# Kernel tuning notes

Measured on AMD Instinct MI355X. Metric: run time of the kernel, lower is better.

Reference implementation:

```python
import jax, jax.numpy as jnp
import numpy as np

NUM_Q = 50000
DIM_KEY = 128
DIM_VALUE = 256
DIM_HIDDEN = 512
MEM_SIZE = 50
BATCH = 128
SEQ = 2048


def setup_inputs() -> dict:
    key = jax.random.key(0)
    ks = jax.random.split(key, 12)
    inp = {
        "q": jax.random.randint(ks[0], (BATCH, SEQ), 0, NUM_Q + 1, dtype=jnp.int64 if jax.config.jax_enable_x64 else jnp.int32),
        "a": jax.random.randint(ks[1], (BATCH, SEQ), 0, 2, dtype=jnp.int64 if jax.config.jax_enable_x64 else jnp.int32),
        # learned parameters (torch Linear convention: y = x @ W.T + b)
        "key_memory": jax.random.normal(ks[2], (MEM_SIZE, DIM_KEY), jnp.float32) * 0.1,
        "value_memory": jax.random.normal(ks[3], (MEM_SIZE, DIM_VALUE), jnp.float32) * 0.1,
        "embed_table": jax.random.normal(ks[4], (NUM_Q + 1, DIM_KEY), jnp.float32) * 0.1,
        "W_erase": jax.random.normal(ks[5], (DIM_VALUE, DIM_HIDDEN), jnp.float32) * 0.05,
        "b_erase": jnp.zeros((DIM_VALUE,), jnp.float32),
        "W_add": jax.random.normal(ks[6], (DIM_VALUE, DIM_HIDDEN), jnp.float32) * 0.05,
        "b_add": jnp.zeros((DIM_VALUE,), jnp.float32),
        "W_f": jax.random.normal(ks[7], (DIM_HIDDEN, DIM_VALUE + DIM_KEY), jnp.float32) * 0.05,
        "b_f": jnp.zeros((DIM_HIDDEN,), jnp.float32),
        "W_p": jax.random.normal(ks[8], (1, DIM_HIDDEN), jnp.float32) * 0.05,
        "b_p": jnp.zeros((1,), jnp.float32),
    }
    return inp


def reference(q, a, key_memory, value_memory, embed_table, W_erase, b_erase,
              W_add, b_add, W_f, b_f, W_p, b_p):
    # NOTE: in the original torch module, read() always uses the static
    # value_memory parameter (not the per-batch updated memory), and the
    # answer sequence `a` is never used in the forward math. Hence the
    # timestep loop is embarrassingly parallel and we vectorize over t.
    q_embed = embed_table[q]                                   # [B,S,K]
    corr = jax.nn.softmax(jnp.einsum('bsk,mk->bsm', q_embed, key_memory), axis=-1)  # [B,S,M]
    read_content = jnp.einsum('bsm,mv->bsv', corr, value_memory)                    # [B,S,V]
    feat = jnp.concatenate([read_content, q_embed], axis=-1)   # [B,S,V+K]
    # dropout is identity in eval mode
    state = jax.nn.relu(jnp.einsum('bsf,hf->bsh', feat, W_f) + b_f)                 # [B,S,H]
    pred = jax.nn.sigmoid(jnp.einsum('bsh,oh->bso', state, W_p) + b_p)              # [B,S,1]
    return pred[..., 0]                                        # [B,S]
```

## Files before the change

### kernel.cpp

```cpp
#include <hip/hip_runtime.h>
#include <hip/hip_bf16.h>

#define NUM_Q_MAX 50000
#define DIM_KEY 128
#define DIM_VAL 256
#define WF_COLS 384
#define DIM_HID 512
#define MEMN    50
#define KDIM    192
#define EOFF    56
#define PITCH   200
#define QB      64

typedef __bf16 bf16x8 __attribute__((ext_vector_type(8)));
typedef float  f32x4  __attribute__((ext_vector_type(4)));
union Frag { uint4 u; bf16x8 b; };

__device__ __forceinline__ float blo(unsigned u){ return __uint_as_float(u << 16); }
__device__ __forceinline__ float bhi(unsigned u){ return __uint_as_float(u & 0xffff0000u); }
__device__ __forceinline__ unsigned short f2b(float x){
    unsigned u = __float_as_uint(x);
    u += 0x7fffu + ((u >> 16) & 1u);
    return (unsigned short)(u >> 16);
}
__device__ __forceinline__ unsigned pk2(float a, float b){
    return (unsigned)f2b(a) | ((unsigned)f2b(b) << 16);
}

__global__ void __launch_bounds__(64)
prep_kernel(const float* __restrict__ Wf, const float* __restrict__ Vm,
            const float* __restrict__ Kmem,
            unsigned short* __restrict__ WCt, unsigned short* __restrict__ Kbt){
    const int b = blockIdx.x, t = threadIdx.x;
    if (b < DIM_HID) {
        const int h = b, nt = h >> 4, l15 = h & 15;
        for (int j = t; j < KDIM; j += 64) {
            float val = 0.f;
            if (j < MEMN) {
                const float4* wr = (const float4*)(Wf + h * WF_COLS);
                const float4* vr = (const float4*)(Vm + j * DIM_VAL);
                float s = 0.f;
                for (int v = 0; v < DIM_VAL / 4; ++v) {
                    float4 a = wr[v], c = vr[v];
                    s += a.x*c.x + a.y*c.y + a.z*c.z + a.w*c.w;
                }
                val = s;
            } else if (j >= EOFF && j < EOFF + DIM_KEY) {
                val = Wf[h * WF_COLS + DIM_VAL + (j - EOFF)];
            }
            const int ks = j >> 5, l4 = (j >> 3) & 3, e = j & 7;
            WCt[((nt * 6 + ks) * 64 + l4 * 16 + l15) * 8 + e] = f2b(val);
        }
    } else {
        for (int idx = t; idx < 4 * 4 * 64 * 8; idx += 64) {
            const int e = idx & 7, lane = (idx >> 3) & 63, ks = (idx >> 9) & 3, nt = idx >> 11;
            const int m = nt * 16 + (lane & 15), k = ks * 32 + (lane >> 4) * 8 + e;
            float v = (m < MEMN) ? Kmem[m * DIM_KEY + k] : 0.f;
            Kbt[idx] = f2b(v);
        }
    }
}

__global__ void __launch_bounds__(256, 4)
table_kernel(const float* __restrict__ emb,
             const unsigned short* __restrict__ WCt,
             const unsigned short* __restrict__ Kbt,
             const float* __restrict__ bfv, const float* __restrict__ wpv,
             const float* __restrict__ bpv, float* __restrict__ table){
    __shared__ __align__(16) unsigned short xf[QB * PITCH];
    __shared__ float2 bwl[DIM_HID];
    __shared__ float red[QB][2];
    const int tid  = threadIdx.x;
    const int u0   = blockIdx.x * QB;
    const int lane = tid & 63;
    const int wv   = tid >> 6;
    const int l15  = lane & 15;
    const int l4   = lane >> 4;
    const int mg   = wv & 1;
    const int hg   = wv >> 1;

    int u = u0 + wv * 16 + l15; if (u > NUM_Q_MAX) u = NUM_Q_MAX;
    const float4* ebase = (const float4*)(emb + (long)u * DIM_KEY);
    float4 s0[4], s1[4];
    #pragma unroll
    for (int ks = 0; ks < 4; ++ks) {
        s0[ks] = ebase[ks * 8 + l4 * 2];
        s1[ks] = ebase[ks * 8 + l4 * 2 + 1];
    }
    float bf0 = bfv[tid], wp0 = wpv[tid];
    float bf1 = bfv[tid + 256], wp1 = wpv[tid + 256];
    Frag bk[4][4];
    #pragma unroll
    for (int nt2 = 0; nt2 < 4; ++nt2)
        #pragma unroll
        for (int ks = 0; ks < 4; ++ks)
            bk[nt2][ks].u = *(const uint4*)&Kbt[((nt2 * 4 + ks) * 64 + lane) * 8];

    Frag ef[4];
    #pragma unroll
    for (int ks = 0; ks < 4; ++ks) {
        uint4 w;
        w.x = pk2(s0[ks].x, s0[ks].y); w.y = pk2(s0[ks].z, s0[ks].w);
        w.z = pk2(s1[ks].x, s1[ks].y); w.w = pk2(s1[ks].z, s1[ks].w);
        ef[ks].u = w;
        *(uint4*)&xf[(wv * 16 + l15) * PITCH + EOFF + ks * 32 + l4 * 8] = w;
    }
    if (tid < QB) {
        uint4 z = {0u, 0u, 0u, 0u};
        *(uint4*)&xf[tid * PITCH + EOFF + DIM_KEY] = z;
    }
    bwl[tid]       = make_float2(bf0, wp0);
    bwl[tid + 256] = make_float2(bf1, wp1);

    #pragma unroll
    for (int nt2 = 0; nt2 < 4; ++nt2) {
        f32x4 acc = {0.f, 0.f, 0.f, 0.f};
        #pragma unroll
        for (int ks = 0; ks < 4; ++ks)
            acc = __builtin_amdgcn_mfma_f32_16x16x32_bf16(ef[ks].b, bk[nt2][ks].b, acc, 0, 0, 0);
        const int mcol = nt2 * 16 + l15;
        if (mcol < MEMN) {
            #pragma unroll
            for (int r = 0; r < 4; ++r)
                xf[(wv * 16 + l4 * 4 + r) * PITCH + mcol] = f2b(acc[r]);
        }
    }

    Frag bwA[6], bwB[6];
    #pragma unroll
    for (int ks = 0; ks < 6; ++ks)
        bwA[ks].u = *(const uint4*)&WCt[(((hg * 16) * 6 + ks) * 64 + lane) * 8];

    __syncthreads();

    Frag af[2][6];
    #pragma unroll
    for (int mt = 0; mt < 2; ++mt)
        #pragma unroll
        for (int ks = 2; ks < 6; ++ks)
            af[mt][ks].u = *(const uint4*)&xf[(mg*32 + mt*16 + l15) * PITCH + ks*32 + l4*8];

    {
        const int r = tid >> 2, g = tid & 3;
        unsigned short* rowp = &xf[r * PITCH];
        uint4 v0 = *(const uint4*)&rowp[g * 16];
        uint4 v1 = {0u, 0u, 0u, 0u};
        if (g < 3) v1 = *(const uint4*)&rowp[g * 16 + 8];
        float va[16];
        va[0]=blo(v0.x); va[1]=bhi(v0.x); va[2]=blo(v0.y);  va[3]=bhi(v0.y);
        va[4]=blo(v0.z); va[5]=bhi(v0.z); va[6]=blo(v0.w);  va[7]=bhi(v0.w);
        va[8]=blo(v1.x); va[9]=bhi(v1.x); va[10]=blo(v1.y); va[11]=bhi(v1.y);
        va[12]=blo(v1.z); va[13]=bhi(v1.z); va[14]=blo(v1.w); va[15]=bhi(v1.w);
        const int c0 = g * 16;
        float mx = -1e30f;
        #pragma unroll
        for (int e = 0; e < 16; ++e) if (c0 + e < MEMN) mx = fmaxf(mx, va[e]);
        mx = fmaxf(mx, __shfl_xor(mx, 1, 64));
        mx = fmaxf(mx, __shfl_xor(mx, 2, 64));
        float sum = 0.f;
        #pragma unroll
        for (int e = 0; e < 16; ++e) {
            float ev = (c0 + e < MEMN) ? __expf(va[e] - mx) : 0.f;
            va[e] = ev; sum += ev;
        }
        sum += __shfl_xor(sum, 1, 64);
        sum += __shfl_xor(sum, 2, 64);
        const float inv = 1.f / sum;
        uint4 w0, w1;
        w0.x = pk2(va[0]*inv,  va[1]*inv);  w0.y = pk2(va[2]*inv,  va[3]*inv);
        w0.z = pk2(va[4]*inv,  va[5]*inv);  w0.w = pk2(va[6]*inv,  va[7]*inv);
        *(uint4*)&rowp[g * 16] = w0;
        if (g < 3) {
            w1.x = pk2(va[8]*inv,  va[9]*inv);  w1.y = pk2(va[10]*inv, va[11]*inv);
            w1.z = pk2(va[12]*inv, va[13]*inv); w1.w = pk2(va[14]*inv, va[15]*inv);
            *(uint4*)&rowp[g * 16 + 8] = w1;
        }
    }
    __syncthreads();

    #pragma unroll
    for (int mt = 0; mt < 2; ++mt)
        #pragma unroll
        for (int ks = 0; ks < 2; ++ks)
            af[mt][ks].u = *(const uint4*)&xf[(mg*32 + mt*16 + l15) * PITCH + ks*32 + l4*8];

    const int kseq[6] = {2, 3, 4, 5, 0, 1};
    float psum[2][4] = {{0.f,0.f,0.f,0.f},{0.f,0.f,0.f,0.f}};
    #pragma unroll
    for (int nt = 0; nt < 16; ++nt) {
        Frag* cur = (nt & 1) ? bwB : bwA;
        Frag* nxt = (nt & 1) ? bwA : bwB;
        if (nt < 15) {
            const int g1 = hg * 16 + nt + 1;
            #pragma unroll
            for (int ks = 0; ks < 6; ++ks)
                nxt[ks].u = *(const uint4*)&WCt[((g1 * 6 + ks) * 64 + lane) * 8];
        }
        const float2 bw2 = bwl[hg * 256 + nt * 16 + l15];
        f32x4 acc[2] = {{0.f,0.f,0.f,0.f},{0.f,0.f,0.f,0.f}};
        #pragma unroll
        for (int ksi = 0; ksi < 6; ++ksi) {
            const int ks = kseq[ksi];
            #pragma unroll
            for (int mt = 0; mt < 2; ++mt)
                acc[mt] = __builtin_amdgcn_mfma_f32_16x16x32_bf16(af[mt][ks].b, cur[ks].b, acc[mt], 0, 0, 0);
        }
        #pragma unroll
        for (int mt = 0; mt < 2; ++mt)
            #pragma unroll
            for (int r = 0; r < 4; ++r)
                psum[mt][r] += bw2.y * fmaxf(acc[mt][r] + bw2.x, 0.f);
    }

    #pragma unroll
    for (int off = 1; off < 16; off <<= 1)
        #pragma unroll
        for (int mt = 0; mt < 2; ++mt)
            #pragma unroll
            for (int r = 0; r < 4; ++r)
                psum[mt][r] += __shfl_xor(psum[mt][r], off, 64);

    if (l15 == 0) {
        #pragma unroll
        for (int mt = 0; mt < 2; ++mt)
            #pragma unroll
            for (int r = 0; r < 4; ++r)
                red[mg*32 + mt*16 + l4*4 + r][hg] = psum[mt][r];
    }
    __syncthreads();

    if (tid < QB) {
        float s = red[tid][0] + red[tid][1] + bpv[0];
        float p = 1.f / (1.f + __expf(-s));
        int uo = u0 + tid;
        if (uo <= NUM_Q_MAX) table[uo] = p;
    }
}

__global__ void gather_kernel(const int* __restrict__ q, const float* __restrict__ table,
                              float* __restrict__ out, int n){
    int i = blockIdx.x * 256 + threadIdx.x;
    if (i < n) out[i] = table[q[i]];
}

extern "C" void kernel_launch(void* const* d_in, const int* in_sizes, int n_in,
                              void* d_out, int out_size, void* d_ws, size_t ws_size,
                              hipStream_t stream) {
    const int*   q    = (const int*)  d_in[0];
    const float* Kmem = (const float*)d_in[2];
    const float* Vmem = (const float*)d_in[3];
    const float* emb  = (const float*)d_in[4];
    const float* Wf   = (const float*)d_in[9];
    const float* bf   = (const float*)d_in[10];
    const float* wp   = (const float*)d_in[11];
    const float* bp   = (const float*)d_in[12];
    float* out = (float*)d_out;

    unsigned short* WCt   = (unsigned short*)d_ws;
    unsigned short* Kbt   = (unsigned short*)((char*)d_ws + 196608);
    float*          table = (float*)((char*)d_ws + 196608 + 16384);

    prep_kernel<<<DIM_HID + 1, 64, 0, stream>>>(Wf, Vmem, Kmem, WCt, Kbt);

    int nblk = (NUM_Q_MAX + 1 + QB - 1) / QB;
    table_kernel<<<nblk, 256, 0, stream>>>(emb, WCt, Kbt, bf, wp, bp, table);

    gather_kernel<<<(out_size + 255) / 256, 256, 0, stream>>>(q, table, out, out_size);
}
```

Baseline: 52.21 us.

## Repartition hidden-dim MFMA work so each wave covers all rows with staggered weight loads

```diff
diff --git a/kernel.cpp b/kernel.cpp
--- a/kernel.cpp
+++ b/kernel.cpp
@@ -61,7 +61,7 @@
     }
 }
 
-__global__ void __launch_bounds__(256, 4)
+__global__ void __launch_bounds__(256, 2)
 table_kernel(const float* __restrict__ emb,
              const unsigned short* __restrict__ WCt,
              const unsigned short* __restrict__ Kbt,
@@ -69,15 +69,15 @@
              const float* __restrict__ bpv, float* __restrict__ table){
     __shared__ __align__(16) unsigned short xf[QB * PITCH];
     __shared__ float2 bwl[DIM_HID];
-    __shared__ float red[QB][2];
+    __shared__ float red[QB][4];
     const int tid  = threadIdx.x;
     const int u0   = blockIdx.x * QB;
+    const int bph  = blockIdx.x & 7;
     const int lane = tid & 63;
     const int wv   = tid >> 6;
     const int l15  = lane & 15;
     const int l4   = lane >> 4;
-    const int mg   = wv & 1;
-    const int hg   = wv >> 1;
+    const int wv8  = wv * 8;
 
     int u = u0 + wv * 16 + l15; if (u > NUM_Q_MAX) u = NUM_Q_MAX;
     const float4* ebase = (const float4*)(emb + (long)u * DIM_KEY);
@@ -126,19 +126,26 @@
         }
     }
 
-    Frag bwA[6], bwB[6];
-    #pragma unroll
-    for (int ks = 0; ks < 6; ++ks)
-        bwA[ks].u = *(const uint4*)&WCt[(((hg * 16) * 6 + ks) * 64 + lane) * 8];
+    Frag bw[3][6];
+    {
+        const int g0 = wv8 + (bph & 7);
+        const int g1 = wv8 + ((1 + bph) & 7);
+        #pragma unroll
+        for (int ks = 0; ks < 6; ++ks)
+            bw[0][ks].u = *(const uint4*)&WCt[((g0 * 6 + ks) * 64 + lane) * 8];
+        #pragma unroll
+        for (int ks = 0; ks < 6; ++ks)
+            bw[1][ks].u = *(const uint4*)&WCt[((g1 * 6 + ks) * 64 + lane) * 8];
+    }
 
     __syncthreads();
 
-    Frag af[2][6];
-    #pragma unroll
-    for (int mt = 0; mt < 2; ++mt)
+    Frag af[4][6];
+    #pragma unroll
+    for (int mt = 0; mt < 4; ++mt)
         #pragma unroll
         for (int ks = 2; ks < 6; ++ks)
-            af[mt][ks].u = *(const uint4*)&xf[(mg*32 + mt*16 + l15) * PITCH + ks*32 + l4*8];
+            af[mt][ks].u = *(const uint4*)&xf[(mt*16 + l15) * PITCH + ks*32 + l4*8];
 
     {
         const int r = tid >> 2, g = tid & 3;
@@ -179,34 +186,41 @@
     __syncthreads();
 
     #pragma unroll
-    for (int mt = 0; mt < 2; ++mt)
+    for (int mt = 0; mt < 4; ++mt)
         #pragma unroll
         for (int ks = 0; ks < 2; ++ks)
-            af[mt][ks].u = *(const uint4*)&xf[(mg*32 + mt*16 + l15) * PITCH + ks*32 + l4*8];
+            af[mt][ks].u = *(const uint4*)&xf[(mt*16 + l15) * PITCH + ks*32 + l4*8];
 
     const int kseq[6] = {2, 3, 4, 5, 0, 1};
-    float psum[2][4] = {{0.f,0.f,0.f,0.f},{0.f,0.f,0.f,0.f}};
-    #pragma unroll
-    for (int nt = 0; nt < 16; ++nt) {
-        Frag* cur = (nt & 1) ? bwB : bwA;
-        Frag* nxt = (nt & 1) ? bwA : bwB;
-        if (nt < 15) {
-            const int g1 = hg * 16 + nt + 1;
+    float psum[4][4];
+    #pragma unroll
+    for (int mt = 0; mt < 4; ++mt)
+        #pragma unroll
+        for (int r = 0; r < 4; ++r) psum[mt][r] = 0.f;
+
+    #pragma unroll
+    for (int nti = 0; nti < 8; ++nti) {
+        const int nt = (nti + bph) & 7;
+        const int g  = wv8 + nt;
+        if (nti < 6) {
+            const int gp = wv8 + ((nti + 2 + bph) & 7);
             #pragma unroll
             for (int ks = 0; ks < 6; ++ks)
-                nxt[ks].u = *(const uint4*)&WCt[((g1 * 6 + ks) * 64 + lane) * 8];
-        }
-        const float2 bw2 = bwl[hg * 256 + nt * 16 + l15];
-        f32x4 acc[2] = {{0.f,0.f,0.f,0.f},{0.f,0.f,0.f,0.f}};
+                bw[(nti + 2) % 3][ks].u = *(const uint4*)&WCt[((gp * 6 + ks) * 64 + lane) * 8];
+        }
+        const float2 bw2 = bwl[g * 16 + l15];
+        f32x4 acc[4];
+        #pragma unroll
+        for (int mt = 0; mt < 4; ++mt) acc[mt] = (f32x4){0.f, 0.f, 0.f, 0.f};
         #pragma unroll
         for (int ksi = 0; ksi < 6; ++ksi) {
             const int ks = kseq[ksi];
             #pragma unroll
-            for (int mt = 0; mt < 2; ++mt)
-                acc[mt] = __builtin_amdgcn_mfma_f32_16x16x32_bf16(af[mt][ks].b, cur[ks].b, acc[mt], 0, 0, 0);
-        }
-        #pragma unroll
-        for (int mt = 0; mt < 2; ++mt)
+            for (int mt = 0; mt < 4; ++mt)
+                acc[mt] = __builtin_amdgcn_mfma_f32_16x16x32_bf16(af[mt][ks].b, bw[nti % 3][ks].b, acc[mt], 0, 0, 0);
+        }
+        #pragma unroll
+        for (int mt = 0; mt < 4; ++mt)
             #pragma unroll
             for (int r = 0; r < 4; ++r)
                 psum[mt][r] += bw2.y * fmaxf(acc[mt][r] + bw2.x, 0.f);
@@ -215,22 +229,22 @@
     #pragma unroll
     for (int off = 1; off < 16; off <<= 1)
         #pragma unroll
-        for (int mt = 0; mt < 2; ++mt)
+        for (int mt = 0; mt < 4; ++mt)
             #pragma unroll
             for (int r = 0; r < 4; ++r)
                 psum[mt][r] += __shfl_xor(psum[mt][r], off, 64);
 
     if (l15 == 0) {
         #pragma unroll
-        for (int mt = 0; mt < 2; ++mt)
-            #pragma unroll
-            for (int r = 0; r < 4; ++r)
-                red[mg*32 + mt*16 + l4*4 + r][hg] = psum[mt][r];
+        for (int mt = 0; mt < 4; ++mt)
+            #pragma unroll
+            for (int r = 0; r < 4; ++r)
+                red[mt*16 + l4*4 + r][wv] = psum[mt][r];
     }
     __syncthreads();
 
     if (tid < QB) {
-        float s = red[tid][0] + red[tid][1] + bpv[0];
+        float s = red[tid][0] + red[tid][1] + red[tid][2] + red[tid][3] + bpv[0];
         float p = 1.f / (1.f + __expf(-s));
         int uo = u0 + tid;
         if (uo <= NUM_Q_MAX) table[uo] = p;
```

Result: faster. 48.46 us (-7.2%).
